# Kernel tuning notes

Measured on AMD Instinct MI355X. Metric: run time of the kernel, lower is better.

The kernel has to match this reference:

```python
import jax, jax.numpy as jnp
import numpy as np

K = 512
HIDDEN = 256


def setup_inputs() -> dict:
    key = jax.random.key(0)
    k1, k2 = jax.random.split(key)
    z = jax.random.normal(k1, (8, 8192, HIDDEN), dtype=jnp.float32)
    # codebook init: uniform(-1/k, 1/k) as in the torch module
    codebook = jax.random.uniform(k2, (K, HIDDEN), dtype=jnp.float32,
                                  minval=-1.0 / K, maxval=1.0 / K)
    return {"z": z, "codebook": codebook}


def reference(z, codebook):
    # squared L2 distance to every code, expanded form to avoid the
    # [N, k, hidden] intermediate: ||z||^2 - 2 z.c + ||c||^2
    z2 = jnp.sum(z * z, axis=-1, keepdims=True)            # [B, T, 1]
    c2 = jnp.sum(codebook * codebook, axis=-1)             # [k]
    cross = jnp.einsum('bth,kh->btk', z, codebook)         # [B, T, k]
    distances = z2 - 2.0 * cross + c2                      # [B, T, k]
    ind = jnp.argmin(distances, axis=-1)                   # [B, T] int
    z_q = codebook[ind]                                    # [B, T, hidden]

    vq_loss = jnp.mean((z_q - jax.lax.stop_gradient(z)) ** 2)
    commitment_loss = jnp.mean((z - jax.lax.stop_gradient(z_q)) ** 2)
    z_q_st = z + jax.lax.stop_gradient(z_q - z)
    return (z_q_st, ind, vq_loss + commitment_loss)
```

## Files before the change

kernel.cpp:

```cpp
#include <hip/hip_runtime.h>

#define M_TOKENS 65536
#define HID      256
#define KCODES   512

#define IND_OFF  (M_TOKENS * HID)
#define LOSS_OFF (IND_OFF + M_TOKENS)

#define TAU      1.5e-4f

#define WS_C2_OFF        16
#define WS_BHI_OFF       4096
#define WS_BLO_OFF       (4096 + 262144)
#define WS_LIST_OFF_FAST (4096 + 524288)
#define WS_LIST_OFF_SLOW 4096
#define WS_MIN_FAST      (WS_LIST_OFF_FAST + 8192 * 4)

typedef __attribute__((ext_vector_type(8))) short  short8;
typedef __attribute__((ext_vector_type(4))) float  f32x4;

__device__ inline unsigned short f2bf(float f) {
    unsigned u = __float_as_uint(f);
    u += 0x7FFF + ((u >> 16) & 1);
    return (unsigned short)(u >> 16);
}
__device__ inline float bf2f(unsigned short h) {
    return __uint_as_float(((unsigned)h) << 16);
}

__global__ __launch_bounds__(256) void vq_prep(
    const float* __restrict__ cb,
    unsigned short* __restrict__ Bhi, unsigned short* __restrict__ Blo,
    float* __restrict__ c2, double* __restrict__ acc, int* __restrict__ cnt) {
    int b = blockIdx.x;
    if (b < 64) {
        int g = b * 256 + threadIdx.x;
        int frag = g >> 6, lane = g & 63;
        int nb = frag >> 3, kb = frag & 7;
        int code = nb * 16 + (lane & 15);
        int kk = kb * 32 + (lane >> 4) * 8;
        const float4* s4 = reinterpret_cast<const float4*>(cb + code * HID + kk);
        float4 v0 = s4[0], v1 = s4[1];
        float f[8] = {v0.x, v0.y, v0.z, v0.w, v1.x, v1.y, v1.z, v1.w};
        short8 vh, vl;
        #pragma unroll
        for (int j = 0; j < 8; ++j) {
            unsigned short h = f2bf(f[j]);
            vh[j] = (short)h;
            vl[j] = (short)f2bf(f[j] - bf2f(h));
        }
        *reinterpret_cast<short8*>(Bhi + (size_t)g * 8) = vh;
        *reinterpret_cast<short8*>(Blo + (size_t)g * 8) = vl;
    } else {
        if (b == 64 && threadIdx.x == 0) { *acc = 0.0; *cnt = 0; }
        int k = (b - 64) * 256 + threadIdx.x;
        const float* row = cb + k * HID;
        double s = 0.0;
        for (int i = 0; i < HID; ++i) {
            double v = (double)row[i];
            s = fma(v, v, s);
        }
        c2[k] = (float)s;
    }
}

__global__ __launch_bounds__(256, 4) void vq_main_mfma(
    const float* __restrict__ z, const float* __restrict__ cb,
    const float* __restrict__ c2g,
    const unsigned short* __restrict__ Bhi,
    const unsigned short* __restrict__ Blo,
    float* __restrict__ out, double* __restrict__ loss_acc,
    int* __restrict__ cnt, int* __restrict__ list, int cap) {

    __shared__ short8 ldsB[2][16][64];
    __shared__ float  lds_c2[KCODES];

    const int tid  = threadIdx.x;
    const int wid  = tid >> 6;
    const int lane = tid & 63;
    const int q    = lane >> 4;
    const int tokW = blockIdx.x * 64 + wid * 16;

    const float4* z4  = reinterpret_cast<const float4*>(z);
    const float4* cb4 = reinterpret_cast<const float4*>(cb);

    lds_c2[tid]       = c2g[tid];
    lds_c2[tid + 256] = c2g[tid + 256];

#define STAGE(nbv, bufv) do {                                                  \
        _Pragma("unroll")                                                      \
        for (int j = 0; j < 4; ++j) {                                          \
            int s_  = (wid << 2) | j;                                          \
            int kb_ = s_ & 7;                                                  \
            const unsigned short* src_ =                                       \
                ((s_ < 8) ? Bhi : Blo) +                                       \
                (((size_t)((nbv) * 8 + kb_) * 64 + lane) << 3);                \
            __builtin_amdgcn_global_load_lds(                                  \
                (const __attribute__((address_space(1))) void*)src_,           \
                (__attribute__((address_space(3))) void*)&ldsB[bufv][s_][0],   \
                16, 0, 0);                                                     \
        }                                                                      \
    } while (0)

    STAGE(0, 0);

    short8 ah[8], al[8];
    float sq;
    {
        int token = tokW + (lane & 15);
        const float4* zr = z4 + (size_t)token * 64 + q * 2;
        float s = 0.f;
        #pragma unroll
        for (int kb = 0; kb < 8; ++kb) {
            float4 v0 = zr[kb * 8];
            float4 v1 = zr[kb * 8 + 1];
            float f[8] = {v0.x, v0.y, v0.z, v0.w, v1.x, v1.y, v1.z, v1.w};
            short8 vh, vl;
            #pragma unroll
            for (int j = 0; j < 8; ++j) {
                unsigned short h = f2bf(f[j]);
                vh[j] = (short)h;
                vl[j] = (short)f2bf(f[j] - bf2f(h));
                s = fmaf(f[j], f[j], s);
            }
            ah[kb] = vh;
            al[kb] = vl;
        }
        s += __shfl_xor(s, 16, 64);
        s += __shfl_xor(s, 32, 64);
        sq = s;
    }

    float b1[4], b2[4];
    int   i1[4];
    #pragma unroll
    for (int r = 0; r < 4; ++r) { b1[r] = 3.4e38f; b2[r] = 3.4e38f; i1[r] = 0; }

    for (int k = 0; k < 32; ++k) {
        int buf = k & 1;
        __syncthreads();
        if (k < 31) STAGE(k + 1, buf ^ 1);

        f32x4 aA = {0.f, 0.f, 0.f, 0.f};
        f32x4 aB = {0.f, 0.f, 0.f, 0.f};
        __builtin_amdgcn_s_setprio(1);
        #pragma unroll
        for (int kb = 0; kb < 8; kb += 2) {
            short8 vbh0 = ldsB[buf][kb][lane];
            short8 vbl0 = ldsB[buf][8 + kb][lane];
            short8 vbh1 = ldsB[buf][kb + 1][lane];
            short8 vbl1 = ldsB[buf][8 + kb + 1][lane];
            aA = __builtin_amdgcn_mfma_f32_16x16x32_bf16(ah[kb], vbh0, aA, 0, 0, 0);
            aB = __builtin_amdgcn_mfma_f32_16x16x32_bf16(ah[kb + 1], vbh1, aB, 0, 0, 0);
            aA = __builtin_amdgcn_mfma_f32_16x16x32_bf16(al[kb], vbh0, aA, 0, 0, 0);
            aB = __builtin_amdgcn_mfma_f32_16x16x32_bf16(al[kb + 1], vbh1, aB, 0, 0, 0);
            aA = __builtin_amdgcn_mfma_f32_16x16x32_bf16(ah[kb], vbl0, aA, 0, 0, 0);
            aB = __builtin_amdgcn_mfma_f32_16x16x32_bf16(ah[kb + 1], vbl1, aB, 0, 0, 0);
        }
        __builtin_amdgcn_s_setprio(0);
        int code = k * 16 + (lane & 15);
        float c2v = lds_c2[code];
        #pragma unroll
        for (int r = 0; r < 4; ++r) {
            float s0 = fmaf(-2.f, aA[r] + aB[r], c2v);
            if (s0 < b1[r]) { b2[r] = b1[r]; b1[r] = s0; i1[r] = code; }
            else if (s0 < b2[r]) b2[r] = s0;
        }
    }
#undef STAGE

    #pragma unroll
    for (int st = 1; st <= 8; st <<= 1) {
        #pragma unroll
        for (int r = 0; r < 4; ++r) {
            float ob1 = __shfl_xor(b1[r], st, 64);
            int   oi1 = __shfl_xor(i1[r], st, 64);
            float ob2 = __shfl_xor(b2[r], st, 64);
            if (ob1 < b1[r] || (ob1 == b1[r] && oi1 < i1[r])) {
                b2[r] = fminf(b1[r], ob2);
                b1[r] = ob1;
                i1[r] = oi1;
            } else {
                b2[r] = fminf(b2[r], ob1);
            }
        }
    }

    if ((lane & 15) == 0) {
        float4 iv;
        #pragma unroll
        for (int r = 0; r < 4; ++r) {
            ((float*)&iv)[r] = (float)i1[r];
            if (b2[r] - b1[r] <= TAU) {
                int pos = atomicAdd(cnt, 1);
                if (pos < cap) list[pos] = tokW + q * 4 + r;
            }
        }
        *reinterpret_cast<float4*>(out + IND_OFF + tokW + q * 4) = iv;
    }

    double lsum = 0.0;
    #pragma unroll
    for (int r = 0; r < 4; ++r) {
        float z2r = __shfl(sq, (lane & 48) | (q * 4 + r), 64);
        if ((lane & 15) == 0) lsum += (double)z2r + (double)b1[r];
    }
    lsum += __shfl_xor(lsum, 16, 64);
    lsum += __shfl_xor(lsum, 32, 64);
    if (lane == 0) atomicAdd(loss_acc, lsum);

    float4* out4 = reinterpret_cast<float4*>(out);
    #pragma unroll
    for (int tt = 0; tt < 16; ++tt) {
        int code = __shfl(i1[tt & 3], (tt >> 2) * 16, 64);
        float4 cv = cb4[(size_t)code * 64 + lane];
        out4[(size_t)(tokW + tt) * 64 + lane] = cv;
    }
}

#define BM   128
#define NC   128
#define KS   32
#define PAD  33

__global__ void vq_init(const float* __restrict__ cb, float* __restrict__ c2,
                        double* __restrict__ acc, int* __restrict__ cnt) {
    int k = threadIdx.x;
    if (k == 0) { *acc = 0.0; *cnt = 0; }
    const float* row = cb + k * HID;
    double s = 0.0;
    for (int i = 0; i < HID; ++i) {
        double v = (double)row[i];
        s = fma(v, v, s);
    }
    c2[k] = (float)s;
}

__global__ __launch_bounds__(256, 2) void vq_main_f32(
    const float* __restrict__ z, const float* __restrict__ cb,
    const float* __restrict__ c2g, float* __restrict__ out,
    double* __restrict__ loss_acc, int* __restrict__ cnt,
    int* __restrict__ list, int cap) {

    __shared__ float smem[(BM + NC) * PAD];
    float* zs = smem;
    float* cs = smem + BM * PAD;

    const int tid = threadIdx.x;
    const int tx = tid & 15;
    const int ty = tid >> 4;
    const int tokBase = blockIdx.x * BM;

    const float4* z4g  = reinterpret_cast<const float4*>(z);
    const float4* cb4g = reinterpret_cast<const float4*>(cb);

    float bs[8], bs2[8];
    int   bi[8];
    #pragma unroll
    for (int m = 0; m < 8; ++m) { bs[m] = 3.4e38f; bs2[m] = 3.4e38f; bi[m] = 0; }

    for (int chunk = 0; chunk < KCODES / NC; ++chunk) {
        float acc[8][8];
        #pragma unroll
        for (int m = 0; m < 8; ++m)
            #pragma unroll
            for (int n = 0; n < 8; ++n) acc[m][n] = 0.f;

        for (int ks = 0; ks < HID / KS; ++ks) {
            __syncthreads();
            #pragma unroll
            for (int i = 0; i < 4; ++i) {
                int f   = tid + i * 256;
                int row = f >> 3;
                int k4  = f & 7;
                float4 zv = z4g[(tokBase + row) * (HID / 4) + ks * (KS / 4) + k4];
                int b = row * PAD + k4 * 4;
                zs[b + 0] = zv.x; zs[b + 1] = zv.y; zs[b + 2] = zv.z; zs[b + 3] = zv.w;
                float4 cv = cb4g[(chunk * NC + row) * (HID / 4) + ks * (KS / 4) + k4];
                cs[b + 0] = cv.x; cs[b + 1] = cv.y; cs[b + 2] = cv.z; cs[b + 3] = cv.w;
            }
            __syncthreads();

            #pragma unroll 2
            for (int k = 0; k < KS; ++k) {
                float zf[8], cf[8];
                #pragma unroll
                for (int m = 0; m < 8; ++m) zf[m] = zs[(ty * 8 + m) * PAD + k];
                #pragma unroll
                for (int n = 0; n < 8; ++n) cf[n] = cs[(tx * 8 + n) * PAD + k];
                #pragma unroll
                for (int m = 0; m < 8; ++m)
                    #pragma unroll
                    for (int n = 0; n < 8; ++n)
                        acc[m][n] = fmaf(zf[m], cf[n], acc[m][n]);
            }
        }

        #pragma unroll
        for (int n = 0; n < 8; ++n) {
            int code = chunk * NC + tx * 8 + n;
            float c2v = c2g[code];
            #pragma unroll
            for (int m = 0; m < 8; ++m) {
                float s = fmaf(-2.f, acc[m][n], c2v);
                if (s < bs[m]) { bs2[m] = bs[m]; bs[m] = s; bi[m] = code; }
                else if (s < bs2[m]) bs2[m] = s;
            }
        }
    }

    __syncthreads();
    float* rs   = smem;
    int*   ri   = reinterpret_cast<int*>(smem + BM * 16);
    float* rs2  = smem + BM * 32;
    int*   inds = reinterpret_cast<int*>(smem + BM * 48);
    float* wred = smem + BM * 48 + BM;

    #pragma unroll
    for (int m = 0; m < 8; ++m) {
        int tok = ty * 8 + m;
        rs [tok * 16 + tx] = bs[m];
        ri [tok * 16 + tx] = bi[m];
        rs2[tok * 16 + tx] = bs2[m];
    }
    __syncthreads();

    if (tid < BM) {
        float B1 = rs[tid * 16];
        int   I1 = ri[tid * 16];
        float B2 = rs2[tid * 16];
        for (int j = 1; j < 16; ++j) {
            float b1v = rs [tid * 16 + j];
            int   i1v = ri [tid * 16 + j];
            float b2v = rs2[tid * 16 + j];
            if (b1v < B1 || (b1v == B1 && i1v < I1)) {
                B2 = fminf(B1, b2v); B1 = b1v; I1 = i1v;
            } else {
                B2 = fminf(B2, b1v);
            }
        }
        inds[tid] = I1;
        out[IND_OFF + tokBase + tid] = (float)I1;
        if (B2 - B1 <= TAU) {
            int pos = atomicAdd(cnt, 1);
            if (pos < cap) list[pos] = tokBase + tid;
        }
    }
    __syncthreads();

    float loc = 0.f;
    float4* out4 = reinterpret_cast<float4*>(out);
    for (int it = 0; it < (BM * HID / 4) / 256; ++it) {
        int e4  = it * 256 + tid;
        int tok = e4 >> 6;
        int h4  = e4 & 63;
        int code = inds[tok];
        float4 cv = cb4g[code * 64 + h4];
        float4 zv = z4g[(tokBase + tok) * 64 + h4];
        out4[(tokBase + tok) * 64 + h4] = cv;
        float dx = cv.x - zv.x, dy = cv.y - zv.y;
        float dz = cv.z - zv.z, dw = cv.w - zv.w;
        loc = fmaf(dx, dx, loc);
        loc = fmaf(dy, dy, loc);
        loc = fmaf(dz, dz, loc);
        loc = fmaf(dw, dw, loc);
    }
    #pragma unroll
    for (int off = 32; off > 0; off >>= 1) loc += __shfl_xor(loc, off, 64);
    int wave = tid >> 6;
    if ((tid & 63) == 0) wred[wave] = loc;
    __syncthreads();
    if (tid == 0) {
        double t = (double)wred[0] + (double)wred[1] +
                   (double)wred[2] + (double)wred[3];
        atomicAdd(loss_acc, t);
    }
}

#define RT 8
__global__ __launch_bounds__(256) void vq_refine(
    const float* __restrict__ z, const float* __restrict__ cb,
    const float* __restrict__ c2g, const double* __restrict__ loss_acc,
    const int* __restrict__ cnt, const int* __restrict__ list,
    float* __restrict__ out, int cap) {

    if (blockIdx.x == 0 && threadIdx.x == 0)
        out[LOSS_OFF] = (float)(2.0 * (*loss_acc) / (double)(M_TOKENS * HID));

    __shared__ float  zrow[RT][HID];
    __shared__ double redd[RT][256];
    __shared__ int    redi[RT][256];

    const int tid = threadIdx.x;
    int n = *cnt; if (n > cap) n = cap;

    for (int base = blockIdx.x * RT; base < n; base += gridDim.x * RT) {
        int toks[RT];
        #pragma unroll
        for (int t = 0; t < RT; ++t) {
            int ii = base + t;
            if (ii > n - 1) ii = n - 1;
            toks[t] = list[ii];
        }
        #pragma unroll
        for (int t = 0; t < RT; ++t) {
            float v = z[(size_t)toks[t] * HID + tid];
            zrow[t][tid] = v;
            redd[t][tid] = (double)v * (double)v;
        }
        __syncthreads();
        for (int s = 128; s > 0; s >>= 1) {
            if (tid < s) {
                #pragma unroll
                for (int t = 0; t < RT; ++t) redd[t][tid] += redd[t][tid + s];
            }
            __syncthreads();
        }
        float z2f[RT];
        #pragma unroll
        for (int t = 0; t < RT; ++t) z2f[t] = (float)redd[t][0];
        __syncthreads();

        double bd[RT];
        int    bk[RT];
        #pragma unroll
        for (int t = 0; t < RT; ++t) { bd[t] = 1e300; bk[t] = 1 << 30; }

        for (int c = 0; c < 2; ++c) {
            int k = tid + c * 256;
            const float4* cr = reinterpret_cast<const float4*>(cb + (size_t)k * HID);
            double acc[RT];
            #pragma unroll
            for (int t = 0; t < RT; ++t) acc[t] = 0.0;
            for (int i = 0; i < HID / 4; ++i) {
                float4 cv = cr[i];
                #pragma unroll
                for (int t = 0; t < RT; ++t) {
                    float4 zv = *reinterpret_cast<const float4*>(&zrow[t][i * 4]);
                    acc[t] = fma((double)zv.x, (double)cv.x, acc[t]);
                    acc[t] = fma((double)zv.y, (double)cv.y, acc[t]);
                    acc[t] = fma((double)zv.z, (double)cv.z, acc[t]);
                    acc[t] = fma((double)zv.w, (double)cv.w, acc[t]);
                }
            }
            float c2v = c2g[k];
            #pragma unroll
            for (int t = 0; t < RT; ++t) {
                float cross32 = (float)acc[t];
                float u = 2.0f * cross32;
                float tq = (float)((double)z2f[t] - (double)u);
                float D = (float)((double)tq + (double)c2v);
                double Dd = (double)D;
                if (Dd < bd[t] || (Dd == bd[t] && k < bk[t])) { bd[t] = Dd; bk[t] = k; }
            }
        }
        #pragma unroll
        for (int t = 0; t < RT; ++t) { redd[t][tid] = bd[t]; redi[t][tid] = bk[t]; }
        __syncthreads();
        for (int s = 128; s > 0; s >>= 1) {
            if (tid < s) {
                #pragma unroll
                for (int t = 0; t < RT; ++t) {
                    double d2 = redd[t][tid + s]; int i2 = redi[t][tid + s];
                    if (d2 < redd[t][tid] ||
                        (d2 == redd[t][tid] && i2 < redi[t][tid])) {
                        redd[t][tid] = d2; redi[t][tid] = i2;
                    }
                }
            }
            __syncthreads();
        }
        if (tid < RT) out[IND_OFF + toks[tid]] = (float)redi[tid][0];
        #pragma unroll
        for (int t = 0; t < RT; ++t) {
            int best = redi[t][0];
            out[(size_t)toks[t] * HID + tid] = cb[(size_t)best * HID + tid];
        }
        __syncthreads();
    }
}

extern "C" void kernel_launch(void* const* d_in, const int* in_sizes, int n_in,
                              void* d_out, int out_size, void* d_ws, size_t ws_size,
                              hipStream_t stream) {
    const float* z  = (const float*)d_in[0];
    const float* cb = (const float*)d_in[1];
    float* out = (float*)d_out;
    double* acc = (double*)d_ws;
    int*  cnt = (int*)((char*)d_ws + 8);
    float* c2 = (float*)((char*)d_ws + WS_C2_OFF);

    if (ws_size >= WS_MIN_FAST) {
        unsigned short* Bhi = (unsigned short*)((char*)d_ws + WS_BHI_OFF);
        unsigned short* Blo = (unsigned short*)((char*)d_ws + WS_BLO_OFF);
        int* list = (int*)((char*)d_ws + WS_LIST_OFF_FAST);
        int cap = 8192;
        vq_prep<<<66, 256, 0, stream>>>(cb, Bhi, Blo, c2, acc, cnt);
        vq_main_mfma<<<M_TOKENS / 64, 256, 0, stream>>>(
            z, cb, c2, Bhi, Blo, out, acc, cnt, list, cap);
        vq_refine<<<192, 256, 0, stream>>>(z, cb, c2, acc, cnt, list, out, cap);
    } else {
        int* list = (int*)((char*)d_ws + WS_LIST_OFF_SLOW);
        int cap = 0;
        if (ws_size > WS_LIST_OFF_SLOW + 16) {
            size_t avail = (ws_size - WS_LIST_OFF_SLOW) / 4;
            cap = (avail > 8192) ? 8192 : (int)avail;
        }
        vq_init<<<1, 512, 0, stream>>>(cb, c2, acc, cnt);
        vq_main_f32<<<M_TOKENS / BM, 256, 0, stream>>>(
            z, cb, c2, out, acc, cnt, list, cap);
        vq_refine<<<192, 256, 0, stream>>>(z, cb, c2, acc, cnt, list, out, cap);
    }
}
```

Baseline: 207.1 us.

## Fuse near-tie refinement and loss finalize into MFMA kernel, double tokens per wave

Each wave now handles 32 tokens (two M fragments) that share each staged codebook B fragment, so LDS staging and B reads are amortised over twice the tokens, at the cost of more registers (launch bounds lowered to 2). The main loop tracks the top-3 candidates per token, and near-tie tokens are re-scored in-block in double precision against only those three codes. This replaces the separate vq_refine kernel and its global list and atomic counter. A last-block done counter writes the final loss, removing a launch. The risk is that the true argmin of a near-tie token lies outside the top-3, or that more than 128 tokens are flagged in a block, in which case the extras are silently left unrefined.

Measured after the change: 522.7 us. 152% more time.

```diff
diff --git a/kernel.cpp b/kernel.cpp
--- a/kernel.cpp
+++ b/kernel.cpp
@@ -28,10 +28,23 @@
     return __uint_as_float(((unsigned)h) << 16);
 }
 
+__device__ inline void ins3(float s, int i,
+                            float& b1, int& i1, float& b2, int& i2,
+                            float& b3, int& i3) {
+    if (s < b1 || (s == b1 && i < i1)) {
+        b3 = b2; i3 = i2; b2 = b1; i2 = i1; b1 = s; i1 = i;
+    } else if (s < b2 || (s == b2 && i < i2)) {
+        b3 = b2; i3 = i2; b2 = s; i2 = i;
+    } else if (s < b3 || (s == b3 && i < i3)) {
+        b3 = s; i3 = i;
+    }
+}
+
 __global__ __launch_bounds__(256) void vq_prep(
     const float* __restrict__ cb,
     unsigned short* __restrict__ Bhi, unsigned short* __restrict__ Blo,
-    float* __restrict__ c2, double* __restrict__ acc, int* __restrict__ cnt) {
+    float* __restrict__ c2, double* __restrict__ acc,
+    int* __restrict__ cnt, int* __restrict__ done) {
     int b = blockIdx.x;
     if (b < 64) {
         int g = b * 256 + threadIdx.x;
@@ -52,7 +65,7 @@
         *reinterpret_cast<short8*>(Bhi + (size_t)g * 8) = vh;
         *reinterpret_cast<short8*>(Blo + (size_t)g * 8) = vl;
     } else {
-        if (b == 64 && threadIdx.x == 0) { *acc = 0.0; *cnt = 0; }
+        if (b == 64 && threadIdx.x == 0) { *acc = 0.0; *cnt = 0; *done = 0; }
         int k = (b - 64) * 256 + threadIdx.x;
         const float* row = cb + k * HID;
         double s = 0.0;
@@ -64,22 +77,22 @@
     }
 }
 
-__global__ __launch_bounds__(256, 4) void vq_main_mfma(
+__global__ __launch_bounds__(256, 2) void vq_main_mfma(
     const float* __restrict__ z, const float* __restrict__ cb,
     const float* __restrict__ c2g,
     const unsigned short* __restrict__ Bhi,
     const unsigned short* __restrict__ Blo,
     float* __restrict__ out, double* __restrict__ loss_acc,
-    int* __restrict__ cnt, int* __restrict__ list, int cap) {
-
-    __shared__ short8 ldsB[2][16][64];
+    int* __restrict__ done) {
+
+    __shared__ short8 ldsB[2][32][64];
     __shared__ float  lds_c2[KCODES];
 
     const int tid  = threadIdx.x;
     const int wid  = tid >> 6;
     const int lane = tid & 63;
     const int q    = lane >> 4;
-    const int tokW = blockIdx.x * 64 + wid * 16;
+    const int tokW = blockIdx.x * 128 + wid * 32;
 
     const float4* z4  = reinterpret_cast<const float4*>(z);
     const float4* cb4 = reinterpret_cast<const float4*>(cb);
@@ -87,14 +100,16 @@
     lds_c2[tid]       = c2g[tid];
     lds_c2[tid + 256] = c2g[tid + 256];
 
-#define STAGE(nbv, bufv) do {                                                  \
+#define STAGE(kv, bufv) do {                                                   \
         _Pragma("unroll")                                                      \
-        for (int j = 0; j < 4; ++j) {                                          \
-            int s_  = (wid << 2) | j;                                          \
-            int kb_ = s_ & 7;                                                  \
+        for (int j = 0; j < 8; ++j) {                                          \
+            int s_  = (wid << 3) | j;                                          \
+            int g_  = s_ >> 4;                                                 \
+            int t_  = s_ & 15;                                                 \
+            int kb_ = t_ & 7;                                                  \
             const unsigned short* src_ =                                       \
-                ((s_ < 8) ? Bhi : Blo) +                                       \
-                (((size_t)((nbv) * 8 + kb_) * 64 + lane) << 3);                \
+                ((t_ < 8) ? Bhi : Blo) +                                       \
+                (((size_t)((2 * (kv) + g_) * 8 + kb_) * 64 + lane) << 3);      \
             __builtin_amdgcn_global_load_lds(                                  \
                 (const __attribute__((address_space(1))) void*)src_,           \
                 (__attribute__((address_space(3))) void*)&ldsB[bufv][s_][0],   \
@@ -104,10 +119,11 @@
 
     STAGE(0, 0);
 
-    short8 ah[8], al[8];
-    float sq;
-    {
-        int token = tokW + (lane & 15);
+    short8 ah[2][8], al[2][8];
+    float sq[2];
+    #pragma unroll
+    for (int mf = 0; mf < 2; ++mf) {
+        int token = tokW + mf * 16 + (lane & 15);
         const float4* zr = z4 + (size_t)token * 64 + q * 2;
         float s = 0.f;
         #pragma unroll
@@ -123,98 +139,184 @@
                 vl[j] = (short)f2bf(f[j] - bf2f(h));
                 s = fmaf(f[j], f[j], s);
             }
-            ah[kb] = vh;
-            al[kb] = vl;
+            ah[mf][kb] = vh;
+            al[mf][kb] = vl;
         }
         s += __shfl_xor(s, 16, 64);
         s += __shfl_xor(s, 32, 64);
-        sq = s;
-    }
-
-    float b1[4], b2[4];
-    int   i1[4];
-    #pragma unroll
-    for (int r = 0; r < 4; ++r) { b1[r] = 3.4e38f; b2[r] = 3.4e38f; i1[r] = 0; }
-
-    for (int k = 0; k < 32; ++k) {
+        sq[mf] = s;
+    }
+
+    float b1[2][4], b2[2][4], b3[2][4];
+    int   i1[2][4], i2[2][4], i3[2][4];
+    #pragma unroll
+    for (int mf = 0; mf < 2; ++mf)
+        #pragma unroll
+        for (int r = 0; r < 4; ++r) {
+            b1[mf][r] = 3.4e38f; b2[mf][r] = 3.4e38f; b3[mf][r] = 3.4e38f;
+            i1[mf][r] = 0; i2[mf][r] = 0; i3[mf][r] = 0;
+        }
+
+    #pragma unroll 2
+    for (int k = 0; k < 16; ++k) {
         int buf = k & 1;
         __syncthreads();
-        if (k < 31) STAGE(k + 1, buf ^ 1);
-
-        f32x4 aA = {0.f, 0.f, 0.f, 0.f};
-        f32x4 aB = {0.f, 0.f, 0.f, 0.f};
-        __builtin_amdgcn_s_setprio(1);
-        #pragma unroll
-        for (int kb = 0; kb < 8; kb += 2) {
-            short8 vbh0 = ldsB[buf][kb][lane];
-            short8 vbl0 = ldsB[buf][8 + kb][lane];
-            short8 vbh1 = ldsB[buf][kb + 1][lane];
-            short8 vbl1 = ldsB[buf][8 + kb + 1][lane];
-            aA = __builtin_amdgcn_mfma_f32_16x16x32_bf16(ah[kb], vbh0, aA, 0, 0, 0);
-            aB = __builtin_amdgcn_mfma_f32_16x16x32_bf16(ah[kb + 1], vbh1, aB, 0, 0, 0);
-            aA = __builtin_amdgcn_mfma_f32_16x16x32_bf16(al[kb], vbh0, aA, 0, 0, 0);
-            aB = __builtin_amdgcn_mfma_f32_16x16x32_bf16(al[kb + 1], vbh1, aB, 0, 0, 0);
-            aA = __builtin_amdgcn_mfma_f32_16x16x32_bf16(ah[kb], vbl0, aA, 0, 0, 0);
-            aB = __builtin_amdgcn_mfma_f32_16x16x32_bf16(ah[kb + 1], vbl1, aB, 0, 0, 0);
-        }
-        __builtin_amdgcn_s_setprio(0);
-        int code = k * 16 + (lane & 15);
-        float c2v = lds_c2[code];
+        if (k < 15) STAGE(k + 1, buf ^ 1);
+
+        #pragma unroll
+        for (int g = 0; g < 2; ++g) {
+            f32x4 a0 = {0.f, 0.f, 0.f, 0.f};
+            f32x4 a1 = {0.f, 0.f, 0.f, 0.f};
+            __builtin_amdgcn_s_setprio(1);
+            #pragma unroll
+            for (int kb = 0; kb < 8; ++kb) {
+                short8 vbh = ldsB[buf][g * 16 + kb][lane];
+                short8 vbl = ldsB[buf][g * 16 + 8 + kb][lane];
+                a0 = __builtin_amdgcn_mfma_f32_16x16x32_bf16(ah[0][kb], vbh, a0, 0, 0, 0);
+                a1 = __builtin_amdgcn_mfma_f32_16x16x32_bf16(ah[1][kb], vbh, a1, 0, 0, 0);
+                a0 = __builtin_amdgcn_mfma_f32_16x16x32_bf16(al[0][kb], vbh, a0, 0, 0, 0);
+                a1 = __builtin_amdgcn_mfma_f32_16x16x32_bf16(al[1][kb], vbh, a1, 0, 0, 0);
+                a0 = __builtin_amdgcn_mfma_f32_16x16x32_bf16(ah[0][kb], vbl, a0, 0, 0, 0);
+                a1 = __builtin_amdgcn_mfma_f32_16x16x32_bf16(ah[1][kb], vbl, a1, 0, 0, 0);
+            }
+            __builtin_amdgcn_s_setprio(0);
+            int code = (2 * k + g) * 16 + (lane & 15);
+            float c2v = lds_c2[code];
+            #pragma unroll
+            for (int r = 0; r < 4; ++r) {
+                float s0 = fmaf(-2.f, a0[r], c2v);
+                ins3(s0, code, b1[0][r], i1[0][r], b2[0][r], i2[0][r], b3[0][r], i3[0][r]);
+                float s1 = fmaf(-2.f, a1[r], c2v);
+                ins3(s1, code, b1[1][r], i1[1][r], b2[1][r], i2[1][r], b3[1][r], i3[1][r]);
+            }
+        }
+    }
+#undef STAGE
+
+    char*   sbase = (char*)(&ldsB[0][0][0]);
+    int*    flg   = (int*)sbase;
+    int*    fcnt  = (int*)(sbase + 2048);
+    double* wred  = (double*)(sbase + 2056);
+    int*    bslot = (int*)(sbase + 2184);
+
+    __syncthreads();
+    if (tid == 0) *fcnt = 0;
+
+    #pragma unroll
+    for (int st = 1; st <= 8; st <<= 1) {
+        #pragma unroll
+        for (int mf = 0; mf < 2; ++mf)
+            #pragma unroll
+            for (int r = 0; r < 4; ++r) {
+                float o1 = __shfl_xor(b1[mf][r], st, 64);
+                int   j1 = __shfl_xor(i1[mf][r], st, 64);
+                float o2 = __shfl_xor(b2[mf][r], st, 64);
+                int   j2 = __shfl_xor(i2[mf][r], st, 64);
+                float o3 = __shfl_xor(b3[mf][r], st, 64);
+                int   j3 = __shfl_xor(i3[mf][r], st, 64);
+                ins3(o1, j1, b1[mf][r], i1[mf][r], b2[mf][r], i2[mf][r], b3[mf][r], i3[mf][r]);
+                ins3(o2, j2, b1[mf][r], i1[mf][r], b2[mf][r], i2[mf][r], b3[mf][r], i3[mf][r]);
+                ins3(o3, j3, b1[mf][r], i1[mf][r], b2[mf][r], i2[mf][r], b3[mf][r], i3[mf][r]);
+            }
+    }
+    __syncthreads();
+
+    if ((lane & 15) == 0) {
+        #pragma unroll
+        for (int mf = 0; mf < 2; ++mf) {
+            float4 iv;
+            #pragma unroll
+            for (int r = 0; r < 4; ++r) {
+                ((float*)&iv)[r] = (float)i1[mf][r];
+                if (b2[mf][r] - b1[mf][r] <= TAU) {
+                    int pos = atomicAdd(fcnt, 1);
+                    if (pos < 128) {
+                        flg[pos * 4 + 0] = tokW + mf * 16 + q * 4 + r;
+                        flg[pos * 4 + 1] = i1[mf][r];
+                        flg[pos * 4 + 2] = i2[mf][r];
+                        flg[pos * 4 + 3] = i3[mf][r];
+                    }
+                }
+            }
+            *reinterpret_cast<float4*>(out + IND_OFF + tokW + mf * 16 + q * 4) = iv;
+        }
+    }
+
+    double lsum = 0.0;
+    #pragma unroll
+    for (int mf = 0; mf < 2; ++mf)
         #pragma unroll
         for (int r = 0; r < 4; ++r) {
-            float s0 = fmaf(-2.f, aA[r] + aB[r], c2v);
-            if (s0 < b1[r]) { b2[r] = b1[r]; b1[r] = s0; i1[r] = code; }
-            else if (s0 < b2[r]) b2[r] = s0;
-        }
-    }
-#undef STAGE
-
-    #pragma unroll
-    for (int st = 1; st <= 8; st <<= 1) {
-        #pragma unroll
-        for (int r = 0; r < 4; ++r) {
-            float ob1 = __shfl_xor(b1[r], st, 64);
-            int   oi1 = __shfl_xor(i1[r], st, 64);
-            float ob2 = __shfl_xor(b2[r], st, 64);
-            if (ob1 < b1[r] || (ob1 == b1[r] && oi1 < i1[r])) {
-                b2[r] = fminf(b1[r], ob2);
-                b1[r] = ob1;
-                i1[r] = oi1;
-            } else {
-                b2[r] = fminf(b2[r], ob1);
-            }
-        }
-    }
-
-    if ((lane & 15) == 0) {
-        float4 iv;
-        #pragma unroll
-        for (int r = 0; r < 4; ++r) {
-            ((float*)&iv)[r] = (float)i1[r];
-            if (b2[r] - b1[r] <= TAU) {
-                int pos = atomicAdd(cnt, 1);
-                if (pos < cap) list[pos] = tokW + q * 4 + r;
-            }
-        }
-        *reinterpret_cast<float4*>(out + IND_OFF + tokW + q * 4) = iv;
-    }
-
-    double lsum = 0.0;
-    #pragma unroll
-    for (int r = 0; r < 4; ++r) {
-        float z2r = __shfl(sq, (lane & 48) | (q * 4 + r), 64);
-        if ((lane & 15) == 0) lsum += (double)z2r + (double)b1[r];
-    }
+            float z2r = __shfl(sq[mf], (lane & 48) | (q * 4 + r), 64);
+            if ((lane & 15) == 0) lsum += (double)z2r + (double)b1[mf][r];
+        }
     lsum += __shfl_xor(lsum, 16, 64);
     lsum += __shfl_xor(lsum, 32, 64);
     if (lane == 0) atomicAdd(loss_acc, lsum);
 
     float4* out4 = reinterpret_cast<float4*>(out);
     #pragma unroll
-    for (int tt = 0; tt < 16; ++tt) {
-        int code = __shfl(i1[tt & 3], (tt >> 2) * 16, 64);
+    for (int tt = 0; tt < 32; ++tt) {
+        int code = __shfl(i1[tt >> 4][tt & 3], ((tt >> 2) & 3) * 16, 64);
         float4 cv = cb4[(size_t)code * 64 + lane];
         out4[(size_t)(tokW + tt) * 64 + lane] = cv;
+    }
+
+    __syncthreads();
+    int n = *fcnt; if (n > 128) n = 128;
+    for (int f = 0; f < n; ++f) {
+        int tok  = flg[f * 4 + 0];
+        int c0   = flg[f * 4 + 1];
+        int c1   = flg[f * 4 + 2];
+        int c2i  = flg[f * 4 + 3];
+        float zi = z[(size_t)tok * HID + tid];
+        double p0 = (double)zi * (double)zi;
+        double p1 = (double)zi * (double)cb[(size_t)c0 * HID + tid];
+        double p2 = (double)zi * (double)cb[(size_t)c1 * HID + tid];
+        double p3 = (double)zi * (double)cb[(size_t)c2i * HID + tid];
+        #pragma unroll
+        for (int off = 1; off < 64; off <<= 1) {
+            p0 += __shfl_xor(p0, off, 64);
+            p1 += __shfl_xor(p1, off, 64);
+            p2 += __shfl_xor(p2, off, 64);
+            p3 += __shfl_xor(p3, off, 64);
+        }
+        if (lane == 0) {
+            wred[wid * 4 + 0] = p0; wred[wid * 4 + 1] = p1;
+            wred[wid * 4 + 2] = p2; wred[wid * 4 + 3] = p3;
+        }
+        __syncthreads();
+        if (tid == 0) {
+            double dz2 = wred[0] + wred[4] + wred[8] + wred[12];
+            float z2f = (float)dz2;
+            int cand[3] = {c0, c1, c2i};
+            float bD = 0.f; int bK = -1;
+            #pragma unroll
+            for (int j = 0; j < 3; ++j) {
+                double dc = wred[1 + j] + wred[5 + j] + wred[9 + j] + wred[13 + j];
+                float cross32 = (float)dc;
+                float u = 2.0f * cross32;
+                float tq = (float)((double)z2f - (double)u);
+                float D = (float)((double)tq + (double)lds_c2[cand[j]]);
+                int kk = cand[j];
+                if (bK < 0 || D < bD || (D == bD && kk < bK)) { bD = D; bK = kk; }
+            }
+            *bslot = bK;
+            out[IND_OFF + tok] = (float)bK;
+        }
+        __syncthreads();
+        int best = *bslot;
+        out[(size_t)tok * HID + tid] = cb[(size_t)best * HID + tid];
+        __syncthreads();
+    }
+
+    if (tid == 0) {
+        __threadfence();
+        int d = atomicAdd(done, 1);
+        if (d == (int)gridDim.x - 1) {
+            double v = atomicAdd(loss_acc, 0.0);
+            out[LOSS_OFF] = (float)(2.0 * v / (double)M_TOKENS / (double)HID);
+        }
     }
 }
 
@@ -461,10 +563,10 @@
             if (tid < s) {
                 #pragma unroll
                 for (int t = 0; t < RT; ++t) {
-                    double d2 = redd[t][tid + s]; int i2 = redi[t][tid + s];
+                    double d2 = redd[t][tid + s]; int i2v = redi[t][tid + s];
                     if (d2 < redd[t][tid] ||
-                        (d2 == redd[t][tid] && i2 < redi[t][tid])) {
-                        redd[t][tid] = d2; redi[t][tid] = i2;
+                        (d2 == redd[t][tid] && i2v < redi[t][tid])) {
+                        redd[t][tid] = d2; redi[t][tid] = i2v;
                     }
                 }
             }
@@ -487,18 +589,16 @@
     const float* cb = (const float*)d_in[1];
     float* out = (float*)d_out;
     double* acc = (double*)d_ws;
-    int*  cnt = (int*)((char*)d_ws + 8);
-    float* c2 = (float*)((char*)d_ws + WS_C2_OFF);
+    int*  cnt  = (int*)((char*)d_ws + 8);
+    int*  done = (int*)((char*)d_ws + 12);
+    float* c2  = (float*)((char*)d_ws + WS_C2_OFF);
 
     if (ws_size >= WS_MIN_FAST) {
         unsigned short* Bhi = (unsigned short*)((char*)d_ws + WS_BHI_OFF);
         unsigned short* Blo = (unsigned short*)((char*)d_ws + WS_BLO_OFF);
-        int* list = (int*)((char*)d_ws + WS_LIST_OFF_FAST);
-        int cap = 8192;
-        vq_prep<<<66, 256, 0, stream>>>(cb, Bhi, Blo, c2, acc, cnt);
-        vq_main_mfma<<<M_TOKENS / 64, 256, 0, stream>>>(
-            z, cb, c2, Bhi, Blo, out, acc, cnt, list, cap);
-        vq_refine<<<192, 256, 0, stream>>>(z, cb, c2, acc, cnt, list, out, cap);
+        vq_prep<<<66, 256, 0, stream>>>(cb, Bhi, Blo, c2, acc, cnt, done);
+        vq_main_mfma<<<M_TOKENS / 128, 256, 0, stream>>>(
+            z, cb, c2, Bhi, Blo, out, acc, done);
     } else {
         int* list = (int*)((char*)d_ws + WS_LIST_OFF_SLOW);
         int cap = 0;
```
